# Optimization experiments

Measured on AMD Instinct MI355X. Metric: run time of the kernel, lower is better.

The kernel has to match this reference:

```python
import jax, jax.numpy as jnp
import numpy as np

TAO = 1.0
EPS = 1e-8


def setup_inputs() -> dict:
    key = jax.random.key(0)
    k1, k2, k3 = jax.random.split(key, 3)
    B, S, H = 32, 64, 256
    tmap = jax.random.normal(k1, (B, S, S, H), dtype=jnp.float32)
    pos_query = jax.random.normal(k2, (B, H), dtype=jnp.float32)
    r = jax.random.uniform(k3, (B, S, S))
    mask2d_pos = r < 0.05
    mask2d_neg = (r >= 0.05) & (r < 0.35)
    return {"pos_query": pos_query, "tmap": tmap,
            "mask2d_pos": mask2d_pos, "mask2d_neg": mask2d_neg}


def reference(pos_query, tmap, mask2d_pos, mask2d_neg):
    # Original loops over batch, gathers variable-length pos/neg sets, normalizes
    # twice (once without eps, once with eps inside sim()), then InfoNCE-style loss.
    # Vectorized: compute similarities for ALL (i,j) cells once, reduce with masks.
    u = tmap / jnp.linalg.norm(tmap, axis=-1, keepdims=True)          # pos/neg normalize (no eps)
    u = u / (jnp.linalg.norm(u, axis=-1, keepdims=True) + EPS)        # renormalize inside sim() (with eps)
    q = pos_query / (jnp.linalg.norm(pos_query, axis=-1, keepdims=True) + EPS)
    s = jnp.einsum('bijh,bh->bij', u, q)                              # cosine sims (B,S,S)
    e = jnp.exp(s / TAO)
    num = jnp.sum(e * mask2d_pos, axis=(1, 2))                        # sum exp(pos_sim/tao)
    den = num + jnp.sum(e * mask2d_neg, axis=(1, 2))                  # + sum exp(neg_sim/tao)
    li = -jnp.log(num / (den + EPS))                                  # per-sample loss (B,)
    # original skips samples with empty pos or neg set, averages over the rest
    valid = jnp.any(mask2d_pos, axis=(1, 2)) & jnp.any(mask2d_neg, axis=(1, 2))
    n_valid = jnp.maximum(jnp.sum(valid), 1)
    return jnp.sum(jnp.where(valid, li, 0.0)) / n_valid
```

## Files before the change

### kernel.cpp

```cpp
#include <hip/hip_runtime.h>
#include <math.h>

#define EPSF 1e-8f
constexpr int B = 32;
constexpr int S = 64;
constexpr int H = 256;
constexpr int H4 = H / 4;
constexpr int CELLS_PER_BATCH = S * S;
constexpr int CELLS = B * CELLS_PER_BATCH;
constexpr int CELLS_PER_WAVE = 32;
constexpr int WAVES_PER_BLOCK = 4;
constexpr int CELLS_PER_BLOCK = CELLS_PER_WAVE * WAVES_PER_BLOCK;
constexpr int BLOCKS_PER_BATCH = CELLS_PER_BATCH / CELLS_PER_BLOCK;
constexpr int GRID = CELLS / CELLS_PER_BLOCK;


__global__ __launch_bounds__(256) void main_kernel(const float* __restrict__ tmap,
                                                   const float* __restrict__ pq,
                                                   const int* __restrict__ mask_pos,
                                                   const int* __restrict__ mask_neg,
                                                   float* __restrict__ ws) {
    int tid = threadIdx.x;
    int lane = tid & 63;
    int wid = tid >> 6;
    int b   = blockIdx.x >> 5;
    int sub = blockIdx.x & 31;
    int waveBase = blockIdx.x * CELLS_PER_BLOCK + wid * CELLS_PER_WAVE;

    int p = lane & 15;
    int g = lane >> 4;

    const float4* q4 = (const float4*)pq + (size_t)b * H4;
    float4 qm0 = q4[p], qm1 = q4[p + 16], qm2 = q4[p + 32], qm3 = q4[p + 48];

    float ssq = qm0.x*qm0.x + qm0.y*qm0.y + qm0.z*qm0.z + qm0.w*qm0.w
              + qm1.x*qm1.x + qm1.y*qm1.y + qm1.z*qm1.z + qm1.w*qm1.w
              + qm2.x*qm2.x + qm2.y*qm2.y + qm2.z*qm2.z + qm2.w*qm2.w
              + qm3.x*qm3.x + qm3.y*qm3.y + qm3.z*qm3.z + qm3.w*qm3.w;
    #pragma unroll
    for (int off = 1; off <= 8; off <<= 1) ssq += __shfl_xor(ssq, off);
    float scale = (1.0f / (sqrtf(ssq) + EPSF)) * (1.0f / (1.0f + EPSF));

    int mp = 0, mn = 0;
    if (lane < CELLS_PER_WAVE) {
        mp = mask_pos[waveBase + lane];
        mn = mask_neg[waveBase + lane];
    }
    unsigned bp = (unsigned)__ballot(mp != 0);
    unsigned bn = (unsigned)__ballot(mn != 0);
    unsigned rem = bp | bn;

    const float4* t4 = (const float4*)tmap;
    float wp = 0.0f, wn = 0.0f;

    while (rem) {
        int k0 = __ffs(rem) - 1; rem &= rem - 1;
        int k1 = -1, k2 = -1, k3 = -1;
        if (rem) { k1 = __ffs(rem) - 1; rem &= rem - 1;
            if (rem) { k2 = __ffs(rem) - 1; rem &= rem - 1;
                if (rem) { k3 = __ffs(rem) - 1; rem &= rem - 1; } } }
        int kg = (g == 0) ? k0 : (g == 1) ? k1 : (g == 2) ? k2 : k3;
        if (kg >= 0) {
            const float4* cp = t4 + (size_t)(waveBase + kg) * H4 + p;
            float4 t0 = cp[0], t1 = cp[16], t2 = cp[32], t3 = cp[48];
            float d  = t0.x*qm0.x + t0.y*qm0.y + t0.z*qm0.z + t0.w*qm0.w
                     + t1.x*qm1.x + t1.y*qm1.y + t1.z*qm1.z + t1.w*qm1.w
                     + t2.x*qm2.x + t2.y*qm2.y + t2.z*qm2.z + t2.w*qm2.w
                     + t3.x*qm3.x + t3.y*qm3.y + t3.z*qm3.z + t3.w*qm3.w;
            float ss = t0.x*t0.x + t0.y*t0.y + t0.z*t0.z + t0.w*t0.w
                     + t1.x*t1.x + t1.y*t1.y + t1.z*t1.z + t1.w*t1.w
                     + t2.x*t2.x + t2.y*t2.y + t2.z*t2.z + t2.w*t2.w
                     + t3.x*t3.x + t3.y*t3.y + t3.z*t3.z + t3.w*t3.w;
            #pragma unroll
            for (int off = 1; off <= 8; off <<= 1) {
                d  += __shfl_xor(d, off);
                ss += __shfl_xor(ss, off);
            }
            float s = d * scale * rsqrtf(ss);
            float e = __expf(s);
            if ((bp >> kg) & 1) wp += e;
            if ((bn >> kg) & 1) wn += e;
        }
    }

    wp += __shfl_xor(wp, 16); wp += __shfl_xor(wp, 32);
    wn += __shfl_xor(wn, 16); wn += __shfl_xor(wn, 32);

    __shared__ float sp[WAVES_PER_BLOCK], sn[WAVES_PER_BLOCK];
    if (lane == 0) { sp[wid] = wp; sn[wid] = wn; }
    __syncthreads();
    if (tid == 0) {
        float tp = sp[0] + sp[1] + sp[2] + sp[3];
        float tn = sn[0] + sn[1] + sn[2] + sn[3];
        ((float2*)ws)[sub * B + b] = make_float2(tp, tn);
    }
}

__global__ __launch_bounds__(256) void final_kernel(const float* __restrict__ ws,
                                                    float* __restrict__ out) {
    const float2* pp = (const float2*)ws;
    int tid = threadIdx.x;
    int lane = tid & 63, w = tid >> 6;
    int b = w * 8 + (lane >> 3);
    int h = lane & 7;
    float ep = 0.0f, en = 0.0f;
    #pragma unroll
    for (int m = 0; m < 4; ++m) {
        float2 v = pp[(h + 8 * m) * B + b];
        ep += v.x; en += v.y;
    }
    #pragma unroll
    for (int off = 1; off <= 4; off <<= 1) {
        ep += __shfl_xor(ep, off);
        en += __shfl_xor(en, off);
    }
    __shared__ float2 acc[B];
    if (h == 0) acc[b] = make_float2(ep, en);
    __syncthreads();
    if (tid < B) {
        float2 a = acc[tid];
        float li = 0.0f; int v = 0;
        if (a.x > 0.0f && a.y > 0.0f) {
            v = 1;
            li = -logf(a.x / (a.x + a.y + EPSF));
        }
        #pragma unroll
        for (int off = 16; off > 0; off >>= 1) {
            li += __shfl_xor(li, off);
            v  += __shfl_xor(v, off);
        }
        if (tid == 0) out[0] = li / (float)(v > 0 ? v : 1);
    }
}

extern "C" void kernel_launch(void* const* d_in, const int* in_sizes, int n_in,
                              void* d_out, int out_size, void* d_ws, size_t ws_size,
                              hipStream_t stream) {
    const float* pos_query = (const float*)d_in[0];
    const float* tmap      = (const float*)d_in[1];
    const int*   mask_pos  = (const int*)d_in[2];
    const int*   mask_neg  = (const int*)d_in[3];
    float* out = (float*)d_out;
    float* ws  = (float*)d_ws;

    main_kernel<<<GRID, 256, 0, stream>>>(tmap, pos_query, mask_pos, mask_neg, ws);
    final_kernel<<<1, 256, 0, stream>>>(ws, out);
}
```

Measured before the change: 184.7 us.

## Use one-wave blocks and double-buffer masked cell loads

The main kernel now launches one 64-thread block per wave of 32 cells and writes per-wave partial sums directly, so the shared-memory reduction and block barrier are gone. The final kernel sums 128 partials per batch instead of 32. The gather loop is software-pipelined with two register buffers, so the next group of four masked cells is loaded while the current group is reduced, aiming to hide memory latency. This raises register pressure and the number of blocks launched.

```diff
diff --git a/kernel.cpp b/kernel.cpp
--- a/kernel.cpp
+++ b/kernel.cpp
@@ -9,23 +9,32 @@
 constexpr int CELLS_PER_BATCH = S * S;
 constexpr int CELLS = B * CELLS_PER_BATCH;
 constexpr int CELLS_PER_WAVE = 32;
-constexpr int WAVES_PER_BLOCK = 4;
-constexpr int CELLS_PER_BLOCK = CELLS_PER_WAVE * WAVES_PER_BLOCK;
-constexpr int BLOCKS_PER_BATCH = CELLS_PER_BATCH / CELLS_PER_BLOCK;
-constexpr int GRID = CELLS / CELLS_PER_BLOCK;
+constexpr int NWAVES = CELLS / CELLS_PER_WAVE;
+constexpr int WAVES_PER_BATCH = CELLS_PER_BATCH / CELLS_PER_WAVE;
 
 
-__global__ __launch_bounds__(256) void main_kernel(const float* __restrict__ tmap,
-                                                   const float* __restrict__ pq,
-                                                   const int* __restrict__ mask_pos,
-                                                   const int* __restrict__ mask_neg,
-                                                   float* __restrict__ ws) {
-    int tid = threadIdx.x;
-    int lane = tid & 63;
-    int wid = tid >> 6;
-    int b   = blockIdx.x >> 5;
-    int sub = blockIdx.x & 31;
-    int waveBase = blockIdx.x * CELLS_PER_BLOCK + wid * CELLS_PER_WAVE;
+__device__ inline int pickg(unsigned& rem, int g) {
+    int k = -1;
+    #pragma unroll
+    for (int i = 0; i < 4; ++i) {
+        if (rem) {
+            int kk = __ffs(rem) - 1;
+            rem &= rem - 1;
+            if (i == g) k = kk;
+        }
+    }
+    return k;
+}
+
+__global__ __launch_bounds__(64) void main_kernel(const float* __restrict__ tmap,
+                                                  const float* __restrict__ pq,
+                                                  const int* __restrict__ mask_pos,
+                                                  const int* __restrict__ mask_neg,
+                                                  float* __restrict__ ws) {
+    int lane = threadIdx.x;
+    int wave = blockIdx.x;
+    int b = wave / WAVES_PER_BATCH;
+    int waveBase = wave * CELLS_PER_WAVE;
 
     int p = lane & 15;
     int g = lane >> 4;
@@ -48,65 +57,73 @@
     }
     unsigned bp = (unsigned)__ballot(mp != 0);
     unsigned bn = (unsigned)__ballot(mn != 0);
-    unsigned rem = bp | bn;
+    unsigned act = bp | bn;
 
     const float4* t4 = (const float4*)tmap;
     float wp = 0.0f, wn = 0.0f;
 
-    while (rem) {
-        int k0 = __ffs(rem) - 1; rem &= rem - 1;
-        int k1 = -1, k2 = -1, k3 = -1;
-        if (rem) { k1 = __ffs(rem) - 1; rem &= rem - 1;
-            if (rem) { k2 = __ffs(rem) - 1; rem &= rem - 1;
-                if (rem) { k3 = __ffs(rem) - 1; rem &= rem - 1; } } }
-        int kg = (g == 0) ? k0 : (g == 1) ? k1 : (g == 2) ? k2 : k3;
-        if (kg >= 0) {
-            const float4* cp = t4 + (size_t)(waveBase + kg) * H4 + p;
-            float4 t0 = cp[0], t1 = cp[16], t2 = cp[32], t3 = cp[48];
-            float d  = t0.x*qm0.x + t0.y*qm0.y + t0.z*qm0.z + t0.w*qm0.w
-                     + t1.x*qm1.x + t1.y*qm1.y + t1.z*qm1.z + t1.w*qm1.w
-                     + t2.x*qm2.x + t2.y*qm2.y + t2.z*qm2.z + t2.w*qm2.w
-                     + t3.x*qm3.x + t3.y*qm3.y + t3.z*qm3.z + t3.w*qm3.w;
-            float ss = t0.x*t0.x + t0.y*t0.y + t0.z*t0.z + t0.w*t0.w
-                     + t1.x*t1.x + t1.y*t1.y + t1.z*t1.z + t1.w*t1.w
-                     + t2.x*t2.x + t2.y*t2.y + t2.z*t2.z + t2.w*t2.w
-                     + t3.x*t3.x + t3.y*t3.y + t3.z*t3.z + t3.w*t3.w;
-            #pragma unroll
-            for (int off = 1; off <= 8; off <<= 1) {
-                d  += __shfl_xor(d, off);
-                ss += __shfl_xor(ss, off);
-            }
-            float s = d * scale * rsqrtf(ss);
-            float e = __expf(s);
-            if ((bp >> kg) & 1) wp += e;
-            if ((bn >> kg) & 1) wn += e;
+#define LOADC(kv, r0, r1, r2, r3)                                          \
+    if (kv >= 0) {                                                         \
+        const float4* cp = t4 + (size_t)(waveBase + kv) * H4 + p;          \
+        r0 = cp[0]; r1 = cp[16]; r2 = cp[32]; r3 = cp[48];                 \
+    }
+
+#define PROCESS(kv, r0, r1, r2, r3)                                        \
+    if (kv >= 0) {                                                         \
+        float d  = r0.x*qm0.x + r0.y*qm0.y + r0.z*qm0.z + r0.w*qm0.w       \
+                 + r1.x*qm1.x + r1.y*qm1.y + r1.z*qm1.z + r1.w*qm1.w       \
+                 + r2.x*qm2.x + r2.y*qm2.y + r2.z*qm2.z + r2.w*qm2.w       \
+                 + r3.x*qm3.x + r3.y*qm3.y + r3.z*qm3.z + r3.w*qm3.w;      \
+        float ss = r0.x*r0.x + r0.y*r0.y + r0.z*r0.z + r0.w*r0.w           \
+                 + r1.x*r1.x + r1.y*r1.y + r1.z*r1.z + r1.w*r1.w           \
+                 + r2.x*r2.x + r2.y*r2.y + r2.z*r2.z + r2.w*r2.w           \
+                 + r3.x*r3.x + r3.y*r3.y + r3.z*r3.z + r3.w*r3.w;          \
+        _Pragma("unroll")                                                  \
+        for (int off = 1; off <= 8; off <<= 1) {                           \
+            d  += __shfl_xor(d, off);                                      \
+            ss += __shfl_xor(ss, off);                                     \
+        }                                                                  \
+        float s = d * scale * rsqrtf(ss);                                  \
+        float e = __expf(s);                                  \
+        if ((bp >> kv) & 1) wp += e;                                       \
+        if ((bn >> kv) & 1) wn += e;                                       \
+    }
+
+    if (act) {
+        unsigned rem = act;
+        float4 a0, a1, a2, a3, c0, c1, c2, c3;
+        int kA = pickg(rem, g);
+        LOADC(kA, a0, a1, a2, a3)
+        bool liveA = true;
+        while (liveA) {
+            bool liveB = (rem != 0);
+            int kB = liveB ? pickg(rem, g) : -1;
+            LOADC(kB, c0, c1, c2, c3)
+            PROCESS(kA, a0, a1, a2, a3)
+            liveA = (rem != 0);
+            kA = liveA ? pickg(rem, g) : -1;
+            LOADC(kA, a0, a1, a2, a3)
+            PROCESS(kB, c0, c1, c2, c3)
         }
     }
+#undef LOADC
+#undef PROCESS
 
     wp += __shfl_xor(wp, 16); wp += __shfl_xor(wp, 32);
     wn += __shfl_xor(wn, 16); wn += __shfl_xor(wn, 32);
-
-    __shared__ float sp[WAVES_PER_BLOCK], sn[WAVES_PER_BLOCK];
-    if (lane == 0) { sp[wid] = wp; sn[wid] = wn; }
-    __syncthreads();
-    if (tid == 0) {
-        float tp = sp[0] + sp[1] + sp[2] + sp[3];
-        float tn = sn[0] + sn[1] + sn[2] + sn[3];
-        ((float2*)ws)[sub * B + b] = make_float2(tp, tn);
-    }
+    if (lane == 0) ((float2*)ws)[wave] = make_float2(wp, wn);
 }
 
 __global__ __launch_bounds__(256) void final_kernel(const float* __restrict__ ws,
                                                     float* __restrict__ out) {
     const float2* pp = (const float2*)ws;
     int tid = threadIdx.x;
-    int lane = tid & 63, w = tid >> 6;
-    int b = w * 8 + (lane >> 3);
-    int h = lane & 7;
+    int b = tid >> 3;
+    int h = tid & 7;
     float ep = 0.0f, en = 0.0f;
     #pragma unroll
-    for (int m = 0; m < 4; ++m) {
-        float2 v = pp[(h + 8 * m) * B + b];
+    for (int m = 0; m < 16; ++m) {
+        float2 v = pp[b * WAVES_PER_BATCH + h + 8 * m];
         ep += v.x; en += v.y;
     }
     #pragma unroll
@@ -143,6 +160,6 @@
     float* out = (float*)d_out;
     float* ws  = (float*)d_ws;
 
-    main_kernel<<<GRID, 256, 0, stream>>>(tmap, pos_query, mask_pos, mask_neg, ws);
+    main_kernel<<<NWAVES, 64, 0, stream>>>(tmap, pos_query, mask_pos, mask_neg, ws);
     final_kernel<<<1, 256, 0, stream>>>(ws, out);
 }
```

After: 185.0 us. No clear change (+0.2%).
